# Performance work log

Hardware: AMD Instinct MI355X
Metric: run time of the kernel (lower is better)

Reference implementation:

```python
import jax, jax.numpy as jnp
import numpy as np


def setup_inputs() -> dict:
    key = jax.random.key(0)
    k1, = jax.random.split(key, 1)
    x = jax.random.normal(k1, (8, 256, 128, 128), dtype=jnp.float32)
    alpha = jnp.ones((1,), dtype=jnp.float32)
    return {"x": x, "alpha": alpha}


def reference(x, alpha):
    B, C, H, W = x.shape
    v = x.reshape(B, C, H * W)                 # [B, C, HW] (query=key=value)
    energy = jnp.einsum('bcs,bds->bcd', v, v)  # [B, C, C]
    # max-softmax: softmax(max(energy) - energy) along last dim
    energy_new = jnp.max(energy, axis=-1, keepdims=True) - energy
    w = jax.nn.softmax(energy_new, axis=-1)    # [B, C, C]
    y = jnp.einsum('bcd,bds->bcs', w, v)       # [B, C, HW]
    y = y.reshape(B, C, H, W)
    return alpha * y + x
```

## Files before the change

kernel.cpp:

```cpp
#include <hip/hip_runtime.h>
#include <math.h>

static constexpr int Bn = 8;
static constexpr int Cn = 256;
static constexpr int Sn = 16384;

typedef __bf16 bf16x4 __attribute__((ext_vector_type(4)));
typedef __bf16 bf16x8 __attribute__((ext_vector_type(8)));
typedef float  f32x4  __attribute__((ext_vector_type(4)));

static constexpr int TILE   = 128;
static constexpr int KSPLIT = 16;
static constexpr int KSLICE = Sn / KSPLIT;
static constexpr int KB     = 32;
static constexpr int LP     = 56;

__global__ __launch_bounds__(256, 2) void gram_kernel(const float* __restrict__ x,
                                                      float* __restrict__ energy) {
  const int b   = blockIdx.z;
  const int tij = blockIdx.y;
  const int ti  = tij >> 1, tj = tij & 1;
  const int kk  = blockIdx.x;

  const float* vb    = x + (size_t)b * Cn * Sn;
  const float* Abase = vb + (size_t)(ti * TILE) * Sn + kk * KSLICE;
  const float* Bbase = vb + (size_t)(tj * TILE) * Sn + kk * KSLICE;

  __shared__ __align__(16) __bf16 Ah[TILE * LP];
  __shared__ __align__(16) __bf16 Al[TILE * LP];
  __shared__ __align__(16) __bf16 Bh[TILE * LP];
  __shared__ __align__(16) __bf16 Bl[TILE * LP];

  const int t    = threadIdx.x;
  const int lane = t & 63;
  const int wv   = t >> 6;
  const int wr   = wv >> 1;
  const int wc   = wv & 1;
  const int ln   = lane & 15;
  const int quad = lane >> 4;

  f32x4 acc[4][4];
#pragma unroll
  for (int i = 0; i < 4; i++)
#pragma unroll
    for (int j = 0; j < 4; j++) acc[i][j] = (f32x4){0.f, 0.f, 0.f, 0.f};

  for (int kc = 0; kc < KSLICE; kc += KB) {
#pragma unroll
    for (int it = 0; it < 4; it++) {
      int idx = t + it * 256;
      int row = idx >> 3;
      int kq  = idx & 7;
      float4 av = *(const float4*)(Abase + (size_t)row * Sn + kc + kq * 4);
      float4 bv = *(const float4*)(Bbase + (size_t)row * Sn + kc + kq * 4);
      bf16x4 ah, al4, bh, bl4;
      {
        __bf16 h0 = (__bf16)av.x, h1 = (__bf16)av.y, h2 = (__bf16)av.z, h3 = (__bf16)av.w;
        ah  = (bf16x4){h0, h1, h2, h3};
        al4 = (bf16x4){(__bf16)(av.x - (float)h0), (__bf16)(av.y - (float)h1),
                       (__bf16)(av.z - (float)h2), (__bf16)(av.w - (float)h3)};
      }
      {
        __bf16 h0 = (__bf16)bv.x, h1 = (__bf16)bv.y, h2 = (__bf16)bv.z, h3 = (__bf16)bv.w;
        bh  = (bf16x4){h0, h1, h2, h3};
        bl4 = (bf16x4){(__bf16)(bv.x - (float)h0), (__bf16)(bv.y - (float)h1),
                       (__bf16)(bv.z - (float)h2), (__bf16)(bv.w - (float)h3)};
      }
      *(bf16x4*)&Ah[row * LP + kq * 4] = ah;
      *(bf16x4*)&Al[row * LP + kq * 4] = al4;
      *(bf16x4*)&Bh[row * LP + kq * 4] = bh;
      *(bf16x4*)&Bl[row * LP + kq * 4] = bl4;
    }
    __syncthreads();

    bf16x8 fah[4], fal[4], fbh[4], fbl[4];
#pragma unroll
    for (int i = 0; i < 4; i++) {
      int ar = wr * 64 + i * 16 + ln;
      int br = wc * 64 + i * 16 + ln;
      fah[i] = *(const bf16x8*)&Ah[ar * LP + quad * 8];
      fal[i] = *(const bf16x8*)&Al[ar * LP + quad * 8];
      fbh[i] = *(const bf16x8*)&Bh[br * LP + quad * 8];
      fbl[i] = *(const bf16x8*)&Bl[br * LP + quad * 8];
    }
#pragma unroll
    for (int i = 0; i < 4; i++)
#pragma unroll
      for (int j = 0; j < 4; j++) {
        acc[i][j] = __builtin_amdgcn_mfma_f32_16x16x32_bf16(fah[i], fbh[j], acc[i][j], 0, 0, 0);
        acc[i][j] = __builtin_amdgcn_mfma_f32_16x16x32_bf16(fah[i], fbl[j], acc[i][j], 0, 0, 0);
        acc[i][j] = __builtin_amdgcn_mfma_f32_16x16x32_bf16(fal[i], fbh[j], acc[i][j], 0, 0, 0);
      }
    __syncthreads();
  }

  float* eb = energy + ((size_t)b * Cn + ti * TILE) * Cn + tj * TILE;
#pragma unroll
  for (int i = 0; i < 4; i++)
#pragma unroll
    for (int j = 0; j < 4; j++) {
      int c0 = wr * 64 + i * 16 + quad * 4;
      int d  = wc * 64 + j * 16 + ln;
#pragma unroll
      for (int r = 0; r < 4; r++)
        atomicAdd(&eb[(size_t)(c0 + r) * Cn + d], acc[i][j][r]);
    }
}

__global__ __launch_bounds__(256) void softmax_kernel(float* __restrict__ energy) {
  const int row = blockIdx.x;
  const int t   = threadIdx.x;
  float e = energy[(size_t)row * Cn + t];

  __shared__ float red[256];
  red[t] = e;
  __syncthreads();
  for (int s = 128; s > 0; s >>= 1) {
    if (t < s) red[t] = fminf(red[t], red[t + s]);
    __syncthreads();
  }
  float emin = red[0];
  __syncthreads();

  float p = expf(emin - e);
  red[t] = p;
  __syncthreads();
  for (int s = 128; s > 0; s >>= 1) {
    if (t < s) red[t] += red[t + s];
    __syncthreads();
  }
  float inv = 1.f / red[0];
  energy[(size_t)row * Cn + t] = p * inv;
}

static constexpr int LPY = 40;

__global__ __launch_bounds__(256, 2) void ygemm_mfma_kernel(const float* __restrict__ w,
                                                            const float* __restrict__ x,
                                                            const float* __restrict__ alpha,
                                                            float* __restrict__ out) {
  const int b  = blockIdx.z;
  const int m0 = blockIdx.y * 128;
  const int s0 = blockIdx.x * 128;

  const float* Wb = w + ((size_t)b * Cn + m0) * Cn;
  const float* Vb = x + (size_t)b * Cn * Sn;

  __shared__ __align__(16) __bf16 Ah[128 * LPY];
  __shared__ __align__(16) __bf16 Al[128 * LPY];
  __shared__ __align__(16) __bf16 Bh[128 * LPY];
  __shared__ __align__(16) __bf16 Bl[128 * LPY];

  const int t    = threadIdx.x;
  const int lane = t & 63;
  const int wv   = t >> 6;
  const int wr   = wv >> 1;
  const int wc   = wv & 1;
  const int ln   = lane & 15;
  const int quad = lane >> 4;

  const int kq8 = t & 7;
  const int sr0 = t >> 3;

  f32x4 acc[4][4];
#pragma unroll
  for (int i = 0; i < 4; i++)
#pragma unroll
    for (int j = 0; j < 4; j++) acc[i][j] = (f32x4){0.f, 0.f, 0.f, 0.f};

  for (int kc = 0; kc < Cn; kc += KB) {
#pragma unroll
    for (int it = 0; it < 4; it++) {
      int idx = t + it * 256;
      int row = idx >> 3;
      int kq  = idx & 7;
      float4 av = *(const float4*)(Wb + (size_t)row * Cn + kc + kq * 4);
      __bf16 h0 = (__bf16)av.x, h1 = (__bf16)av.y, h2 = (__bf16)av.z, h3 = (__bf16)av.w;
      *(bf16x4*)&Ah[row * LPY + kq * 4] = (bf16x4){h0, h1, h2, h3};
      *(bf16x4*)&Al[row * LPY + kq * 4] = (bf16x4){(__bf16)(av.x - (float)h0),
                                                   (__bf16)(av.y - (float)h1),
                                                   (__bf16)(av.z - (float)h2),
                                                   (__bf16)(av.w - (float)h3)};
    }
#pragma unroll
    for (int it = 0; it < 4; it++) {
      int s = sr0 + it * 32;
      const float* col = Vb + (size_t)(kc + kq8 * 4) * Sn + s0 + s;
      float e0 = col[0];
      float e1 = col[(size_t)Sn];
      float e2 = col[(size_t)2 * Sn];
      float e3 = col[(size_t)3 * Sn];
      __bf16 h0 = (__bf16)e0, h1 = (__bf16)e1, h2 = (__bf16)e2, h3 = (__bf16)e3;
      *(bf16x4*)&Bh[s * LPY + kq8 * 4] = (bf16x4){h0, h1, h2, h3};
      *(bf16x4*)&Bl[s * LPY + kq8 * 4] = (bf16x4){(__bf16)(e0 - (float)h0),
                                                  (__bf16)(e1 - (float)h1),
                                                  (__bf16)(e2 - (float)h2),
                                                  (__bf16)(e3 - (float)h3)};
    }
    __syncthreads();

    bf16x8 fah[4], fal[4], fbh[4], fbl[4];
#pragma unroll
    for (int i = 0; i < 4; i++) {
      int ar = wr * 64 + i * 16 + ln;
      int br = wc * 64 + i * 16 + ln;
      fah[i] = *(const bf16x8*)&Ah[ar * LPY + quad * 8];
      fal[i] = *(const bf16x8*)&Al[ar * LPY + quad * 8];
      fbh[i] = *(const bf16x8*)&Bh[br * LPY + quad * 8];
      fbl[i] = *(const bf16x8*)&Bl[br * LPY + quad * 8];
    }
#pragma unroll
    for (int i = 0; i < 4; i++)
#pragma unroll
      for (int j = 0; j < 4; j++) {
        acc[i][j] = __builtin_amdgcn_mfma_f32_16x16x32_bf16(fah[i], fbh[j], acc[i][j], 0, 0, 0);
        acc[i][j] = __builtin_amdgcn_mfma_f32_16x16x32_bf16(fah[i], fbl[j], acc[i][j], 0, 0, 0);
        acc[i][j] = __builtin_amdgcn_mfma_f32_16x16x32_bf16(fal[i], fbh[j], acc[i][j], 0, 0, 0);
      }
    __syncthreads();
  }

  const float al = alpha[0];
#pragma unroll
  for (int i = 0; i < 4; i++)
#pragma unroll
    for (int j = 0; j < 4; j++) {
      int c = m0 + wr * 64 + i * 16 + quad * 4;
      int s = s0 + wc * 64 + j * 16 + ln;
      const float* xr = x   + ((size_t)b * Cn + c) * Sn + s;
      float*       orp = out + ((size_t)b * Cn + c) * Sn + s;
#pragma unroll
      for (int r = 0; r < 4; r++)
        orp[(size_t)r * Sn] = al * acc[i][j][r] + xr[(size_t)r * Sn];
    }
}

extern "C" void kernel_launch(void* const* d_in, const int* in_sizes, int n_in,
                              void* d_out, int out_size, void* d_ws, size_t ws_size,
                              hipStream_t stream) {
  const float* x     = (const float*)d_in[0];
  const float* alpha = (const float*)d_in[1];
  float*       out   = (float*)d_out;
  float*       energy = (float*)d_ws;

  const size_t energy_bytes = (size_t)Bn * Cn * Cn * sizeof(float);
  hipMemsetAsync(energy, 0, energy_bytes, stream);

  dim3 g1(KSPLIT, 4, Bn);
  gram_kernel<<<g1, 256, 0, stream>>>(x, energy);

  softmax_kernel<<<Bn * Cn, 256, 0, stream>>>(energy);

  dim3 g3(Sn / 128, Cn / 128, Bn);
  ygemm_mfma_kernel<<<g3, 256, 0, stream>>>(energy, x, alpha, out);
}
```

Measured before the change: 350.6 us.

## Exploit Gram symmetry, prefetch tiles into registers, swizzle LDS, warp-level softmax

```diff
diff --git a/kernel.cpp b/kernel.cpp
--- a/kernel.cpp
+++ b/kernel.cpp
@@ -8,28 +8,42 @@
 typedef __bf16 bf16x4 __attribute__((ext_vector_type(4)));
 typedef __bf16 bf16x8 __attribute__((ext_vector_type(8)));
 typedef float  f32x4  __attribute__((ext_vector_type(4)));
+
+__device__ __forceinline__ void split_store(__bf16* __restrict__ Hi, __bf16* __restrict__ Lo,
+                                            int row, int kq, float4 v) {
+  __bf16 h0 = (__bf16)v.x, h1 = (__bf16)v.y, h2 = (__bf16)v.z, h3 = (__bf16)v.w;
+  int off = row * 32 + (((kq >> 1) ^ (row & 3)) << 3) + ((kq & 1) << 2);
+  *(bf16x4*)&Hi[off] = (bf16x4){h0, h1, h2, h3};
+  *(bf16x4*)&Lo[off] = (bf16x4){(__bf16)(v.x - (float)h0), (__bf16)(v.y - (float)h1),
+                                (__bf16)(v.z - (float)h2), (__bf16)(v.w - (float)h3)};
+}
+
+__device__ __forceinline__ bf16x8 frag_ld(const __bf16* __restrict__ P, int row, int quad) {
+  return *(const bf16x8*)&P[row * 32 + ((quad ^ (row & 3)) << 3)];
+}
 
 static constexpr int TILE   = 128;
 static constexpr int KSPLIT = 16;
 static constexpr int KSLICE = Sn / KSPLIT;
 static constexpr int KB     = 32;
-static constexpr int LP     = 56;
 
 __global__ __launch_bounds__(256, 2) void gram_kernel(const float* __restrict__ x,
                                                       float* __restrict__ energy) {
-  const int b   = blockIdx.z;
-  const int tij = blockIdx.y;
-  const int ti  = tij >> 1, tj = tij & 1;
-  const int kk  = blockIdx.x;
+  const int b    = blockIdx.z;
+  const int tsel = blockIdx.y;
+  const int kk   = blockIdx.x;
+  const int ti   = (tsel == 1) ? 1 : 0;
+  const int tj   = (tsel == 0) ? 0 : 1;
+  const bool diag = (tsel < 2);
 
   const float* vb    = x + (size_t)b * Cn * Sn;
   const float* Abase = vb + (size_t)(ti * TILE) * Sn + kk * KSLICE;
   const float* Bbase = vb + (size_t)(tj * TILE) * Sn + kk * KSLICE;
 
-  __shared__ __align__(16) __bf16 Ah[TILE * LP];
-  __shared__ __align__(16) __bf16 Al[TILE * LP];
-  __shared__ __align__(16) __bf16 Bh[TILE * LP];
-  __shared__ __align__(16) __bf16 Bl[TILE * LP];
+  __shared__ __align__(16) __bf16 Ah[TILE * 32];
+  __shared__ __align__(16) __bf16 Al[TILE * 32];
+  __shared__ __align__(16) __bf16 Bh[TILE * 32];
+  __shared__ __align__(16) __bf16 Bl[TILE * 32];
 
   const int t    = threadIdx.x;
   const int lane = t & 63;
@@ -39,6 +53,20 @@
   const int ln   = lane & 15;
   const int quad = lane >> 4;
 
+  const int srow = t >> 3;
+  const int skq  = t & 7;
+
+  float4 areg[4], breg[4];
+
+#pragma unroll
+  for (int it = 0; it < 4; it++)
+    areg[it] = *(const float4*)(Abase + (size_t)(srow + it * 32) * Sn + skq * 4);
+  if (!diag) {
+#pragma unroll
+    for (int it = 0; it < 4; it++)
+      breg[it] = *(const float4*)(Bbase + (size_t)(srow + it * 32) * Sn + skq * 4);
+  }
+
   f32x4 acc[4][4];
 #pragma unroll
   for (int i = 0; i < 4; i++)
@@ -47,93 +75,87 @@
 
   for (int kc = 0; kc < KSLICE; kc += KB) {
 #pragma unroll
-    for (int it = 0; it < 4; it++) {
-      int idx = t + it * 256;
-      int row = idx >> 3;
-      int kq  = idx & 7;
-      float4 av = *(const float4*)(Abase + (size_t)row * Sn + kc + kq * 4);
-      float4 bv = *(const float4*)(Bbase + (size_t)row * Sn + kc + kq * 4);
-      bf16x4 ah, al4, bh, bl4;
-      {
-        __bf16 h0 = (__bf16)av.x, h1 = (__bf16)av.y, h2 = (__bf16)av.z, h3 = (__bf16)av.w;
-        ah  = (bf16x4){h0, h1, h2, h3};
-        al4 = (bf16x4){(__bf16)(av.x - (float)h0), (__bf16)(av.y - (float)h1),
-                       (__bf16)(av.z - (float)h2), (__bf16)(av.w - (float)h3)};
-      }
-      {
-        __bf16 h0 = (__bf16)bv.x, h1 = (__bf16)bv.y, h2 = (__bf16)bv.z, h3 = (__bf16)bv.w;
-        bh  = (bf16x4){h0, h1, h2, h3};
-        bl4 = (bf16x4){(__bf16)(bv.x - (float)h0), (__bf16)(bv.y - (float)h1),
-                       (__bf16)(bv.z - (float)h2), (__bf16)(bv.w - (float)h3)};
-      }
-      *(bf16x4*)&Ah[row * LP + kq * 4] = ah;
-      *(bf16x4*)&Al[row * LP + kq * 4] = al4;
-      *(bf16x4*)&Bh[row * LP + kq * 4] = bh;
-      *(bf16x4*)&Bl[row * LP + kq * 4] = bl4;
-    }
-    __syncthreads();
-
-    bf16x8 fah[4], fal[4], fbh[4], fbl[4];
+    for (int it = 0; it < 4; it++) split_store(Ah, Al, srow + it * 32, skq, areg[it]);
+    if (!diag) {
+#pragma unroll
+      for (int it = 0; it < 4; it++) split_store(Bh, Bl, srow + it * 32, skq, breg[it]);
+    }
+    __syncthreads();
+
+    const __bf16* PH = diag ? Ah : Bh;
+    const __bf16* PL = diag ? Al : Bl;
+
+    bf16x8 fah[4], fal[4];
 #pragma unroll
     for (int i = 0; i < 4; i++) {
       int ar = wr * 64 + i * 16 + ln;
-      int br = wc * 64 + i * 16 + ln;
-      fah[i] = *(const bf16x8*)&Ah[ar * LP + quad * 8];
-      fal[i] = *(const bf16x8*)&Al[ar * LP + quad * 8];
-      fbh[i] = *(const bf16x8*)&Bh[br * LP + quad * 8];
-      fbl[i] = *(const bf16x8*)&Bl[br * LP + quad * 8];
-    }
-#pragma unroll
-    for (int i = 0; i < 4; i++)
-#pragma unroll
-      for (int j = 0; j < 4; j++) {
-        acc[i][j] = __builtin_amdgcn_mfma_f32_16x16x32_bf16(fah[i], fbh[j], acc[i][j], 0, 0, 0);
-        acc[i][j] = __builtin_amdgcn_mfma_f32_16x16x32_bf16(fah[i], fbl[j], acc[i][j], 0, 0, 0);
-        acc[i][j] = __builtin_amdgcn_mfma_f32_16x16x32_bf16(fal[i], fbh[j], acc[i][j], 0, 0, 0);
-      }
-    __syncthreads();
-  }
-
-  float* eb = energy + ((size_t)b * Cn + ti * TILE) * Cn + tj * TILE;
-#pragma unroll
-  for (int i = 0; i < 4; i++)
-#pragma unroll
-    for (int j = 0; j < 4; j++) {
-      int c0 = wr * 64 + i * 16 + quad * 4;
-      int d  = wc * 64 + j * 16 + ln;
-#pragma unroll
-      for (int r = 0; r < 4; r++)
-        atomicAdd(&eb[(size_t)(c0 + r) * Cn + d], acc[i][j][r]);
+      fah[i] = frag_ld(Ah, ar, quad);
+      fal[i] = frag_ld(Al, ar, quad);
+    }
+
+    if (kc + KB < KSLICE) {
+#pragma unroll
+      for (int it = 0; it < 4; it++)
+        areg[it] = *(const float4*)(Abase + (size_t)(srow + it * 32) * Sn + (kc + KB) + skq * 4);
+      if (!diag) {
+#pragma unroll
+        for (int it = 0; it < 4; it++)
+          breg[it] = *(const float4*)(Bbase + (size_t)(srow + it * 32) * Sn + (kc + KB) + skq * 4);
+      }
+    }
+
+#pragma unroll
+    for (int j = 0; j < 4; j++) {
+      int br = wc * 64 + j * 16 + ln;
+      bf16x8 fbh = frag_ld(PH, br, quad);
+      bf16x8 fbl = frag_ld(PL, br, quad);
+#pragma unroll
+      for (int i = 0; i < 4; i++) {
+        acc[i][j] = __builtin_amdgcn_mfma_f32_16x16x32_bf16(fah[i], fbh, acc[i][j], 0, 0, 0);
+        acc[i][j] = __builtin_amdgcn_mfma_f32_16x16x32_bf16(fah[i], fbl, acc[i][j], 0, 0, 0);
+        acc[i][j] = __builtin_amdgcn_mfma_f32_16x16x32_bf16(fal[i], fbh, acc[i][j], 0, 0, 0);
+      }
+    }
+    __syncthreads();
+  }
+
+  float* E = energy + (size_t)b * Cn * Cn;
+#pragma unroll
+  for (int i = 0; i < 4; i++)
+#pragma unroll
+    for (int j = 0; j < 4; j++) {
+      int c0 = ti * TILE + wr * 64 + i * 16 + quad * 4;
+      int d  = tj * TILE + wc * 64 + j * 16 + ln;
+#pragma unroll
+      for (int r = 0; r < 4; r++) {
+        float v = acc[i][j][r];
+        atomicAdd(&E[(size_t)(c0 + r) * Cn + d], v);
+        if (tsel == 2) atomicAdd(&E[(size_t)d * Cn + (c0 + r)], v);
+      }
     }
 }
 
 __global__ __launch_bounds__(256) void softmax_kernel(float* __restrict__ energy) {
-  const int row = blockIdx.x;
-  const int t   = threadIdx.x;
-  float e = energy[(size_t)row * Cn + t];
-
-  __shared__ float red[256];
-  red[t] = e;
-  __syncthreads();
-  for (int s = 128; s > 0; s >>= 1) {
-    if (t < s) red[t] = fminf(red[t], red[t + s]);
-    __syncthreads();
-  }
-  float emin = red[0];
-  __syncthreads();
-
-  float p = expf(emin - e);
-  red[t] = p;
-  __syncthreads();
-  for (int s = 128; s > 0; s >>= 1) {
-    if (t < s) red[t] += red[t + s];
-    __syncthreads();
-  }
-  float inv = 1.f / red[0];
-  energy[(size_t)row * Cn + t] = p * inv;
-}
-
-static constexpr int LPY = 40;
+  const int wv   = threadIdx.x >> 6;
+  const int lane = threadIdx.x & 63;
+  const int row  = blockIdx.x * 4 + wv;
+
+  float4 e = *(const float4*)&energy[(size_t)row * Cn + lane * 4];
+  float m = fminf(fminf(e.x, e.y), fminf(e.z, e.w));
+#pragma unroll
+  for (int off = 32; off > 0; off >>= 1) m = fminf(m, __shfl_xor(m, off));
+
+  float4 p;
+  p.x = expf(m - e.x); p.y = expf(m - e.y);
+  p.z = expf(m - e.z); p.w = expf(m - e.w);
+  float s = p.x + p.y + p.z + p.w;
+#pragma unroll
+  for (int off = 32; off > 0; off >>= 1) s += __shfl_xor(s, off);
+
+  float inv = 1.f / s;
+  p.x *= inv; p.y *= inv; p.z *= inv; p.w *= inv;
+  *(float4*)&energy[(size_t)row * Cn + lane * 4] = p;
+}
 
 __global__ __launch_bounds__(256, 2) void ygemm_mfma_kernel(const float* __restrict__ w,
                                                             const float* __restrict__ x,
@@ -146,10 +168,10 @@
   const float* Wb = w + ((size_t)b * Cn + m0) * Cn;
   const float* Vb = x + (size_t)b * Cn * Sn;
 
-  __shared__ __align__(16) __bf16 Ah[128 * LPY];
-  __shared__ __align__(16) __bf16 Al[128 * LPY];
-  __shared__ __align__(16) __bf16 Bh[128 * LPY];
-  __shared__ __align__(16) __bf16 Bl[128 * LPY];
+  __shared__ __align__(16) __bf16 Ah[128 * 32];
+  __shared__ __align__(16) __bf16 Al[128 * 32];
+  __shared__ __align__(16) __bf16 Bh[128 * 32];
+  __shared__ __align__(16) __bf16 Bl[128 * 32];
 
   const int t    = threadIdx.x;
   const int lane = t & 63;
@@ -159,8 +181,23 @@
   const int ln   = lane & 15;
   const int quad = lane >> 4;
 
-  const int kq8 = t & 7;
-  const int sr0 = t >> 3;
+  const int srow = t >> 3;
+  const int skq  = t & 7;
+
+  float4 areg[4];
+  float  breg[16];
+
+#pragma unroll
+  for (int it = 0; it < 4; it++)
+    areg[it] = *(const float4*)(Wb + (size_t)(srow + it * 32) * Cn + skq * 4);
+#pragma unroll
+  for (int it = 0; it < 4; it++) {
+    const float* col = Vb + (size_t)(skq * 4) * Sn + s0 + srow + it * 32;
+    breg[it * 4 + 0] = col[0];
+    breg[it * 4 + 1] = col[(size_t)Sn];
+    breg[it * 4 + 2] = col[(size_t)2 * Sn];
+    breg[it * 4 + 3] = col[(size_t)3 * Sn];
+  }
 
   f32x4 acc[4][4];
 #pragma unroll
@@ -170,53 +207,49 @@
 
   for (int kc = 0; kc < Cn; kc += KB) {
 #pragma unroll
+    for (int it = 0; it < 4; it++) split_store(Ah, Al, srow + it * 32, skq, areg[it]);
+#pragma unroll
     for (int it = 0; it < 4; it++) {
-      int idx = t + it * 256;
-      int row = idx >> 3;
-      int kq  = idx & 7;
-      float4 av = *(const float4*)(Wb + (size_t)row * Cn + kc + kq * 4);
-      __bf16 h0 = (__bf16)av.x, h1 = (__bf16)av.y, h2 = (__bf16)av.z, h3 = (__bf16)av.w;
-      *(bf16x4*)&Ah[row * LPY + kq * 4] = (bf16x4){h0, h1, h2, h3};
-      *(bf16x4*)&Al[row * LPY + kq * 4] = (bf16x4){(__bf16)(av.x - (float)h0),
-                                                   (__bf16)(av.y - (float)h1),
-                                                   (__bf16)(av.z - (float)h2),
-                                                   (__bf16)(av.w - (float)h3)};
-    }
-#pragma unroll
-    for (int it = 0; it < 4; it++) {
-      int s = sr0 + it * 32;
-      const float* col = Vb + (size_t)(kc + kq8 * 4) * Sn + s0 + s;
-      float e0 = col[0];
-      float e1 = col[(size_t)Sn];
-      float e2 = col[(size_t)2 * Sn];
-      float e3 = col[(size_t)3 * Sn];
-      __bf16 h0 = (__bf16)e0, h1 = (__bf16)e1, h2 = (__bf16)e2, h3 = (__bf16)e3;
-      *(bf16x4*)&Bh[s * LPY + kq8 * 4] = (bf16x4){h0, h1, h2, h3};
-      *(bf16x4*)&Bl[s * LPY + kq8 * 4] = (bf16x4){(__bf16)(e0 - (float)h0),
-                                                  (__bf16)(e1 - (float)h1),
-                                                  (__bf16)(e2 - (float)h2),
-                                                  (__bf16)(e3 - (float)h3)};
-    }
-    __syncthreads();
-
-    bf16x8 fah[4], fal[4], fbh[4], fbl[4];
+      float4 bv = make_float4(breg[it * 4 + 0], breg[it * 4 + 1],
+                              breg[it * 4 + 2], breg[it * 4 + 3]);
+      split_store(Bh, Bl, srow + it * 32, skq, bv);
+    }
+    __syncthreads();
+
+    bf16x8 fah[4], fal[4];
 #pragma unroll
     for (int i = 0; i < 4; i++) {
       int ar = wr * 64 + i * 16 + ln;
-      int br = wc * 64 + i * 16 + ln;
-      fah[i] = *(const bf16x8*)&Ah[ar * LPY + quad * 8];
-      fal[i] = *(const bf16x8*)&Al[ar * LPY + quad * 8];
-      fbh[i] = *(const bf16x8*)&Bh[br * LPY + quad * 8];
-      fbl[i] = *(const bf16x8*)&Bl[br * LPY + quad * 8];
-    }
-#pragma unroll
-    for (int i = 0; i < 4; i++)
-#pragma unroll
-      for (int j = 0; j < 4; j++) {
-        acc[i][j] = __builtin_amdgcn_mfma_f32_16x16x32_bf16(fah[i], fbh[j], acc[i][j], 0, 0, 0);
-        acc[i][j] = __builtin_amdgcn_mfma_f32_16x16x32_bf16(fah[i], fbl[j], acc[i][j], 0, 0, 0);
-        acc[i][j] = __builtin_amdgcn_mfma_f32_16x16x32_bf16(fal[i], fbh[j], acc[i][j], 0, 0, 0);
-      }
+      fah[i] = frag_ld(Ah, ar, quad);
+      fal[i] = frag_ld(Al, ar, quad);
+    }
+
+    if (kc + KB < Cn) {
+#pragma unroll
+      for (int it = 0; it < 4; it++)
+        areg[it] = *(const float4*)(Wb + (size_t)(srow + it * 32) * Cn + (kc + KB) + skq * 4);
+#pragma unroll
+      for (int it = 0; it < 4; it++) {
+        const float* col = Vb + (size_t)((kc + KB) + skq * 4) * Sn + s0 + srow + it * 32;
+        breg[it * 4 + 0] = col[0];
+        breg[it * 4 + 1] = col[(size_t)Sn];
+        breg[it * 4 + 2] = col[(size_t)2 * Sn];
+        breg[it * 4 + 3] = col[(size_t)3 * Sn];
+      }
+    }
+
+#pragma unroll
+    for (int j = 0; j < 4; j++) {
+      int br = wc * 64 + j * 16 + ln;
+      bf16x8 fbh = frag_ld(Bh, br, quad);
+      bf16x8 fbl = frag_ld(Bl, br, quad);
+#pragma unroll
+      for (int i = 0; i < 4; i++) {
+        acc[i][j] = __builtin_amdgcn_mfma_f32_16x16x32_bf16(fah[i], fbh, acc[i][j], 0, 0, 0);
+        acc[i][j] = __builtin_amdgcn_mfma_f32_16x16x32_bf16(fah[i], fbl, acc[i][j], 0, 0, 0);
+        acc[i][j] = __builtin_amdgcn_mfma_f32_16x16x32_bf16(fal[i], fbh, acc[i][j], 0, 0, 0);
+      }
+    }
     __syncthreads();
   }
 
@@ -228,10 +261,10 @@
       int c = m0 + wr * 64 + i * 16 + quad * 4;
       int s = s0 + wc * 64 + j * 16 + ln;
       const float* xr = x   + ((size_t)b * Cn + c) * Sn + s;
-      float*       orp = out + ((size_t)b * Cn + c) * Sn + s;
+      float*       op = out + ((size_t)b * Cn + c) * Sn + s;
 #pragma unroll
       for (int r = 0; r < 4; r++)
-        orp[(size_t)r * Sn] = al * acc[i][j][r] + xr[(size_t)r * Sn];
+        op[(size_t)r * Sn] = al * acc[i][j][r] + xr[(size_t)r * Sn];
     }
 }
 
@@ -246,10 +279,10 @@
   const size_t energy_bytes = (size_t)Bn * Cn * Cn * sizeof(float);
   hipMemsetAsync(energy, 0, energy_bytes, stream);
 
-  dim3 g1(KSPLIT, 4, Bn);
+  dim3 g1(KSPLIT, 3, Bn);
   gram_kernel<<<g1, 256, 0, stream>>>(x, energy);
 
-  softmax_kernel<<<Bn * Cn, 256, 0, stream>>>(energy);
+  softmax_kernel<<<(Bn * Cn) / 4, 256, 0, stream>>>(energy);
 
   dim3 g3(Sn / 128, Cn / 128, Bn);
   ygemm_mfma_kernel<<<g3, 256, 0, stream>>>(energy, x, alpha, out);
```

After: 350.7 us. No clear change (+0.0%).
